# Optimization experiments

Hardware: AMD Instinct MI355X
Metric: run time of the kernel (lower is better)

## Reference

```python
import jax, jax.numpy as jnp
import numpy as np


def _cas(N):
    # Hartley cas matrix: cos(2*pi*k*n/N) + sin(2*pi*k*n/N), shape [N, N]
    n = jnp.arange(N, dtype=jnp.float32)
    ang = 2.0 * jnp.pi * n[:, None] * n[None, :] / N
    return jnp.cos(ang) + jnp.sin(ang)


def setup_inputs() -> dict:
    key = jax.random.key(0)
    k0, k1, k2, k3, k4 = jax.random.split(key, 5)
    B, N, C = 8, 4096, 768
    nb, bs, hf = 8, 96, 1
    scale = 0.02
    return {
        "x": jax.random.normal(k0, (B, N, C), jnp.float32),
        "w1": scale * jax.random.normal(k1, (2, nb, bs, bs * hf), jnp.float32),
        "b1": scale * jax.random.normal(k2, (2, nb, bs * hf), jnp.float32),
        "w2": scale * jax.random.normal(k3, (2, nb, bs * hf, bs), jnp.float32),
        "b2": scale * jax.random.normal(k4, (2, nb, bs), jnp.float32),
    }


def reference(x, w1, b1, w2, b2):
    SPARSITY = 0.01       # sparsity_threshold (softshrink lambda)
    FRAC = 1.0            # hard_thresholding_fraction
    B, N, C = x.shape
    H = W = int(np.sqrt(N))
    nb, bs = w1.shape[1], w1.shape[2]
    bias = x

    xf = x.astype(jnp.float32).reshape(B, H, W, C)
    cas = _cas(C)  # module's dht2d transforms the LAST (channel) dim
    xr = xf @ cas  # [B,H,W,C]; imag part is exactly zero after torch.complex(x, 0)
    xr = xr.reshape(B, H, W, nb, bs)

    # kept_modes = int((N//2+1)*frac), clamped by W-dim slicing semantics
    km = min(W, int((N // 2 + 1) * FRAC))

    # block-diagonal 2-layer MLP on (real, imag) with imag input == 0
    o1r = jax.nn.relu(jnp.einsum('bhwki,kio->bhwko', xr, w1[0]) + b1[0])
    o1i = jax.nn.relu(jnp.einsum('bhwki,kio->bhwko', xr, w1[1]) + b1[1])
    o2r = (jnp.einsum('bhwko,koc->bhwkc', o1r, w2[0])
           - jnp.einsum('bhwko,koc->bhwkc', o1i, w2[1]) + b2[0])
    o2i = (jnp.einsum('bhwko,koc->bhwkc', o1i, w2[0])
           + jnp.einsum('bhwko,koc->bhwkc', o1r, w2[1]) + b2[1])

    if km < W:
        mask = (jnp.arange(W) < km)[None, None, :, None, None]
        o2r = jnp.where(mask, o2r, 0.0)
        o2i = jnp.where(mask, o2i, 0.0)

    # softshrink on stacked real/imag
    ss = lambda v: jnp.sign(v) * jnp.maximum(jnp.abs(v) - SPARSITY, 0.0)
    o2r, o2i = ss(o2r), ss(o2i)

    real = o2r.reshape(B, H, W, C)
    imag = o2i.reshape(B, H, W, C)

    # idht2d: dht2d(complex) = real@cas - imag@cas, divided by TOTAL element count
    n_tot = B * H * W * C
    out = ((real - imag) @ cas) / n_tot
    out = out.reshape(B, N, C).astype(bias.dtype)
    return out + bias
```

## Files before the change

kernel.cpp:

```cpp
#include <hip/hip_runtime.h>
#include <hip/hip_bf16.h>
#include <cstdint>
#include <cstddef>

typedef __bf16 bf8_t __attribute__((ext_vector_type(8)));
typedef __bf16 bf4_t __attribute__((ext_vector_type(4)));
typedef float  f4_t  __attribute__((ext_vector_type(4)));

#define CC 768
#define NROWS 32768
#define NTOT 25165824

__device__ __forceinline__ void gld16(const void* g, void* l) {
  __builtin_amdgcn_global_load_lds(
      (const __attribute__((address_space(1))) void*)g,
      (__attribute__((address_space(3))) void*)l, 16, 0, 0);
}


__global__ void make_cas(__bf16* __restrict__ cas) {
  int idx = blockIdx.x * 256 + threadIdx.x;
  int i = idx / CC, j = idx - i * CC;
  int ij = (i * j) % CC;
  float ang = 6.283185307179586f * (float)ij / (float)CC;
  cas[idx] = (__bf16)(__cosf(ang) + __sinf(ang));
}

__global__ void cvt4(const float* __restrict__ x, __bf16* __restrict__ o) {
  int i = (blockIdx.x * 256 + threadIdx.x) * 4;
  float4 v = *(const float4*)(x + i);
  bf4_t r;
  r[0] = (__bf16)v.x; r[1] = (__bf16)v.y; r[2] = (__bf16)v.z; r[3] = (__bf16)v.w;
  *(bf4_t*)(o + i) = r;
}

__global__ void pack_w1(const float* __restrict__ w1, __bf16* __restrict__ w1f) {
  int f = blockIdx.x * 256 + threadIdx.x;
  int j = f & 7, lane = (f >> 3) & 63, rest = f >> 9;
  int nt = rest % 12, kt = (rest / 12) % 3, blk = rest / 36;
  int k = kt * 32 + (lane >> 4) * 8 + j;
  int o = nt * 16 + (lane & 15);
  float v = (o < 96) ? w1[(0 * 8 + blk) * 9216 + k * 96 + o]
                     : w1[(1 * 8 + blk) * 9216 + k * 96 + (o - 96)];
  w1f[f] = (__bf16)v;
}

__global__ void pack_w2(const float* __restrict__ w2, __bf16* __restrict__ w2f) {
  int f = blockIdx.x * 256 + threadIdx.x;
  int j = f & 7, lane = (f >> 3) & 63, rest = f >> 9;
  int nt = rest % 12, kt = (rest / 12) % 6, blk = rest / 72;
  int i = kt * 32 + (lane >> 4) * 8 + j;
  int o = nt * 16 + (lane & 15);
  float v;
  if (o < 96) v = (i < 96) ?  w2[(0 * 8 + blk) * 9216 + i * 96 + o]
                           : -w2[(1 * 8 + blk) * 9216 + (i - 96) * 96 + o];
  else        v = (i < 96) ?  w2[(1 * 8 + blk) * 9216 + i * 96 + (o - 96)]
                           :  w2[(0 * 8 + blk) * 9216 + (i - 96) * 96 + (o - 96)];
  w2f[f] = (__bf16)v;
}

__global__ __launch_bounds__(256, 2) void gemm_back(
    const __bf16* __restrict__ Zb, const __bf16* __restrict__ BT,
    float* __restrict__ Cf, const float* __restrict__ Xres, float scale)
{
  __shared__ __align__(16) char smem[49152];
  const int t = threadIdx.x;
  const int lane = t & 63, wid = t >> 6;
  const int wm = (wid >> 1) * 64, wn = (wid & 1) * 64;

  const int id = blockIdx.x;
  const int sid = (id & 7) * 192 + (id >> 3);
  const int m0 = (sid / 6) * 128, n0 = (sid % 6) * 128;

  const int q = lane >> 4, r = lane & 15;
  const __bf16* gA = Zb + (size_t)(m0 + (t >> 2)) * CC + (t & 3) * 8;
  const __bf16* gB = BT + (size_t)(n0 + (t >> 2)) * CC + (t & 3) * 8;
  const int ldsOff = (t >> 2) * 32 + (t & 3) * 8;

  auto stage = [&](int b, int tile) {
    int k0 = tile * 32;
    __bf16* lA = (__bf16*)(smem + b * 16384) + ldsOff;
    __bf16* lB = (__bf16*)(smem + b * 16384 + 8192) + ldsOff;
    gld16(gA + k0, lA);
    gld16(gA + (size_t)64 * CC + k0, lA + 64 * 32);
    gld16(gB + k0, lB);
    gld16(gB + (size_t)64 * CC + k0, lB + 64 * 32);
  };

  f4_t acc[4][4] = {};
  stage(0, 0);
  stage(1, 1);
  for (int tile = 0; tile < 24; ++tile) {
    int nt = tile + 2; if (nt > 23) nt = 23;
    stage((tile + 2) % 3, nt);
    asm volatile("s_waitcnt vmcnt(8)" ::: "memory");
    __builtin_amdgcn_s_barrier();
    const __bf16* sA = (const __bf16*)(smem + (tile % 3) * 16384);
    const __bf16* sB = sA + 8192 / 2;
    bf8_t af[4], bfr[4];
#pragma unroll
    for (int i = 0; i < 4; i++)
      af[i] = *(const bf8_t*)(sA + (wm + i * 16 + r) * 32 + q * 8);
#pragma unroll
    for (int j = 0; j < 4; j++)
      bfr[j] = *(const bf8_t*)(sB + (wn + j * 16 + r) * 32 + q * 8);
#pragma unroll
    for (int i = 0; i < 4; i++)
#pragma unroll
      for (int j = 0; j < 4; j++)
        acc[i][j] = __builtin_amdgcn_mfma_f32_16x16x32_bf16(af[i], bfr[j], acc[i][j], 0, 0, 0);
    __builtin_amdgcn_s_barrier();
  }

  float* cs = (float*)smem;
#pragma unroll
  for (int h = 0; h < 2; ++h) {
    __builtin_amdgcn_s_barrier();
    if ((wid >> 1) == h) {
#pragma unroll
      for (int i = 0; i < 4; i++)
#pragma unroll
        for (int j = 0; j < 4; j++)
#pragma unroll
          for (int rr = 0; rr < 4; rr++)
            cs[(i * 16 + q * 4 + rr) * 132 + wn + j * 16 + r] = acc[i][j][rr];
    }
    __builtin_amdgcn_s_barrier();
    const int u = t & 31, row8 = t >> 5;
#pragma unroll
    for (int p = 0; p < 8; ++p) {
      int rl = p * 8 + row8;
      size_t goff = (size_t)(m0 + h * 64 + rl) * CC + n0 + u * 4;
      f4_t xr = *(const f4_t*)(Xres + goff);
      f4_t cv = *(const f4_t*)(cs + rl * 132 + u * 4);
      f4_t o;
      o[0] = cv[0] * scale + xr[0];
      o[1] = cv[1] * scale + xr[1];
      o[2] = cv[2] * scale + xr[2];
      o[3] = cv[3] * scale + xr[3];
      *(f4_t*)(Cf + goff) = o;
    }
  }
}

__global__ __launch_bounds__(384, 3) void fused2(
    const __bf16* __restrict__ A, const __bf16* __restrict__ BT,
    const __bf16* __restrict__ w1f, const __bf16* __restrict__ w2f,
    const float* __restrict__ b1, const float* __restrict__ b2,
    __bf16* __restrict__ Z)
{
  __shared__ __align__(16) char smem[63488];
  __bf16* sA = (__bf16*)smem;
  __bf16* sB = (__bf16*)(smem + 8192);
  __bf16* Hs = (__bf16*)smem;
  __bf16* vt = (__bf16*)(smem + 25600);
  __bf16* zl = (__bf16*)(smem + 51200);

  const int t = threadIdx.x, lane = t & 63, w = t >> 6;
  const int id = blockIdx.x;
  const int sid = (id & 7) * 128 + (id >> 3);
  const int cbp = sid & 3;
  const int m0 = (sid >> 2) * 128;
  const int n0 = cbp * 192;
  const int q = lane >> 4, r = lane & 15;

  const __bf16* gA  = A  + (size_t)(m0 + (t >> 2)) * CC + (t & 3) * 8;
  const __bf16* gA2 = A  + (size_t)(m0 + 96 + (t >> 2)) * CC + (t & 3) * 8;
  const __bf16* gB  = BT + (size_t)(n0 + (t >> 2)) * CC + (t & 3) * 8;
  const __bf16* gB2 = BT + (size_t)(n0 + 96 + (t >> 2)) * CC + (t & 3) * 8;
  __bf16* lA  = sA + t * 8;
  __bf16* lA2 = sA + (384 + t) * 8;
  __bf16* lB  = sB + t * 8;
  __bf16* lB2 = sB + (384 + t) * 8;

  f4_t acc[8][2] = {};
  for (int k0 = 0; k0 < CC; k0 += 32) {
    __syncthreads();
    gld16(gA + k0, lA);
    if (t < 128) gld16(gA2 + k0, lA2);
    gld16(gB + k0, lB);
    gld16(gB2 + k0, lB2);
    __syncthreads();
    bf8_t af[8], bfr[2];
#pragma unroll
    for (int i = 0; i < 8; i++)
      af[i] = *(const bf8_t*)(sA + (i * 16 + r) * 32 + q * 8);
#pragma unroll
    for (int j = 0; j < 2; j++)
      bfr[j] = *(const bf8_t*)(sB + (w * 32 + j * 16 + r) * 32 + q * 8);
#pragma unroll
    for (int i = 0; i < 8; i++)
#pragma unroll
      for (int j = 0; j < 2; j++)
        acc[i][j] = __builtin_amdgcn_mfma_f32_16x16x32_bf16(af[i], bfr[j], acc[i][j], 0, 0, 0);
  }

#pragma unroll
  for (int h = 0; h < 2; h++) {
#pragma unroll
    for (int ii = 0; ii < 4; ii++)
#pragma unroll
      for (int j = 0; j < 2; j++) {
        int col = w * 32 + j * 16 + r;
#pragma unroll
        for (int rr = 0; rr < 4; rr++) {
          int row = ii * 16 + q * 4 + rr;
          vt[row * 200 + col] = (__bf16)acc[h * 4 + ii][j][rr];
        }
      }
    __syncthreads();

#pragma unroll
    for (int cb = 0; cb < 2; cb++) {
      const int bidx = cbp * 2 + cb;
      const __bf16* w1b = w1f + (size_t)bidx * (36 * 64 * 8);
      const __bf16* w2b = w2f + (size_t)bidx * (72 * 64 * 8);
      bf8_t w1r[3][2], w2r[6][2];
#pragma unroll
      for (int kt = 0; kt < 3; kt++)
#pragma unroll
        for (int j = 0; j < 2; j++)
          w1r[kt][j] = *(const bf8_t*)(w1b + ((size_t)(kt * 12 + 2 * w + j) * 64 + lane) * 8);
#pragma unroll
      for (int kt = 0; kt < 6; kt++) {
        w2r[kt][0] = *(const bf8_t*)(w2b + ((size_t)(kt * 12 + w) * 64 + lane) * 8);
        w2r[kt][1] = *(const bf8_t*)(w2b + ((size_t)(kt * 12 + w + 6) * 64 + lane) * 8);
      }
      float bb[2];
#pragma unroll
      for (int j = 0; j < 2; j++) {
        int c = (2 * w + j) * 16 + r;
        bb[j] = (c < 96) ? b1[bidx * 96 + c] : b1[768 + bidx * 96 + (c - 96)];
      }
      const float br = b2[bidx * 96 + w * 16 + r];
      const float bi = b2[768 + bidx * 96 + w * 16 + r];

#pragma unroll
      for (int rt = 0; rt < 4; rt++) {
        const __bf16* vp = vt + (rt * 16 + r) * 200 + cb * 96 + q * 8;
        f4_t a0 = {}, a1 = {};
#pragma unroll
        for (int kt = 0; kt < 3; kt++) {
          bf8_t a = *(const bf8_t*)(vp + kt * 32);
          a0 = __builtin_amdgcn_mfma_f32_16x16x32_bf16(a, w1r[kt][0], a0, 0, 0, 0);
          a1 = __builtin_amdgcn_mfma_f32_16x16x32_bf16(a, w1r[kt][1], a1, 0, 0, 0);
        }
#pragma unroll
        for (int j = 0; j < 2; j++) {
          int c = (2 * w + j) * 16 + r;
          f4_t* ap = j ? &a1 : &a0;
#pragma unroll
          for (int rr = 0; rr < 4; rr++) {
            float v = (*ap)[rr] + bb[j];
            Hs[(rt * 16 + q * 4 + rr) * 200 + c] = (__bf16)(v > 0.f ? v : 0.f);
          }
        }
      }
      __syncthreads();
#pragma unroll
      for (int rt = 0; rt < 4; rt++) {
        f4_t ar = {}, ai = {};
#pragma unroll
        for (int kt = 0; kt < 6; kt++) {
          bf8_t a = *(const bf8_t*)(&Hs[(rt * 16 + r) * 200 + kt * 32 + q * 8]);
          ar = __builtin_amdgcn_mfma_f32_16x16x32_bf16(a, w2r[kt][0], ar, 0, 0, 0);
          ai = __builtin_amdgcn_mfma_f32_16x16x32_bf16(a, w2r[kt][1], ai, 0, 0, 0);
        }
#pragma unroll
        for (int rr = 0; rr < 4; rr++) {
          float yr = ar[rr] + br, yi = ai[rr] + bi;
          float sr = fabsf(yr) - 0.01f; sr = sr > 0.f ? copysignf(sr, yr) : 0.f;
          float si = fabsf(yi) - 0.01f; si = si > 0.f ? copysignf(si, yi) : 0.f;
          zl[(rt * 16 + q * 4 + rr) * 96 + w * 16 + r] = (__bf16)(sr - si);
        }
      }
      __syncthreads();
      {
        const uint32_t* zsrc = (const uint32_t*)zl;
        int cdw = t % 48, crow = t / 48;
        int rbase = m0 + h * 64;
#pragma unroll
        for (int it = 0; it < 8; it++) {
          int row = it * 8 + crow;
          uint32_t* dst = (uint32_t*)(Z + (size_t)(rbase + row) * CC + n0 + cb * 96);
          dst[cdw] = zsrc[row * 48 + cdw];
        }
      }
    }
  }
}


extern "C" void kernel_launch(void* const* d_in, const int* in_sizes, int n_in,
                              void* d_out, int out_size, void* d_ws, size_t ws_size,
                              hipStream_t stream) {
  const float* x  = (const float*)d_in[0];
  const float* w1 = (const float*)d_in[1];
  const float* b1 = (const float*)d_in[2];
  const float* w2 = (const float*)d_in[3];
  const float* b2 = (const float*)d_in[4];
  float* out = (float*)d_out;

  char* ws = (char*)d_ws;
  size_t off = 0;
  auto alloc = [&](size_t bytes) {
    char* p = ws + off;
    off += (bytes + 255) & ~(size_t)255;
    return p;
  };
  __bf16* casb = (__bf16*)alloc((size_t)CC * CC * 2);
  __bf16* w1f  = (__bf16*)alloc((size_t)8 * 36 * 64 * 8 * 2);
  __bf16* w2f  = (__bf16*)alloc((size_t)8 * 72 * 64 * 8 * 2);
  __bf16* xb   = (__bf16*)alloc((size_t)NTOT * 2);
  __bf16* vv   = (__bf16*)alloc((size_t)NTOT * 2);

  make_cas<<<2304, 256, 0, stream>>>(casb);
  cvt4<<<24576, 256, 0, stream>>>(x, xb);
  pack_w1<<<576, 256, 0, stream>>>(w1, w1f);
  pack_w2<<<1152, 256, 0, stream>>>(w2, w2f);

  fused2<<<1024, 384, 0, stream>>>(xb, casb, w1f, w2f, b1, b2, vv);
  gemm_back<<<1536, 256, 0, stream>>>(vv, casb, out, x, 1.0f / 25165824.0f);
}
```

Before: 368.5 us.

## Triple-buffer the forward GEMM K-loop with async LDS loads and vmcnt waits

Replaces the single-buffer load/sync/compute loop in the fused forward kernel with a three-stage ring of LDS buffers (20 KB each) filled by global_load_lds two tiles ahead. Explicit s_waitcnt vmcnt thresholds plus raw barriers let the MFMA work on one tile overlap the global loads for later tiles, hiding memory latency. The three buffers fit within the existing 63 KB shared allocation. Redundant reloads of the last tile at the end of the loop and hand-tuned per-wave vmcnt counts add fragility.

Measured after the change: 340.9 us. 7.5% less time.

```diff
diff --git a/kernel.cpp b/kernel.cpp
--- a/kernel.cpp
+++ b/kernel.cpp
@@ -143,15 +143,13 @@
   }
 }
 
-__global__ __launch_bounds__(384, 3) void fused2(
+__global__ __launch_bounds__(384, 3) void fused3(
     const __bf16* __restrict__ A, const __bf16* __restrict__ BT,
     const __bf16* __restrict__ w1f, const __bf16* __restrict__ w2f,
     const float* __restrict__ b1, const float* __restrict__ b2,
     __bf16* __restrict__ Z)
 {
   __shared__ __align__(16) char smem[63488];
-  __bf16* sA = (__bf16*)smem;
-  __bf16* sB = (__bf16*)(smem + 8192);
   __bf16* Hs = (__bf16*)smem;
   __bf16* vt = (__bf16*)(smem + 25600);
   __bf16* zl = (__bf16*)(smem + 51200);
@@ -168,19 +166,27 @@
   const __bf16* gA2 = A  + (size_t)(m0 + 96 + (t >> 2)) * CC + (t & 3) * 8;
   const __bf16* gB  = BT + (size_t)(n0 + (t >> 2)) * CC + (t & 3) * 8;
   const __bf16* gB2 = BT + (size_t)(n0 + 96 + (t >> 2)) * CC + (t & 3) * 8;
-  __bf16* lA  = sA + t * 8;
-  __bf16* lA2 = sA + (384 + t) * 8;
-  __bf16* lB  = sB + t * 8;
-  __bf16* lB2 = sB + (384 + t) * 8;
+
+  auto stage = [&](int b, int tile) {
+    int k0 = tile * 32;
+    char* base = smem + b * 20480;
+    gld16(gA + k0, (__bf16*)base + t * 8);
+    if (t < 128) gld16(gA2 + k0, (__bf16*)base + (384 + t) * 8);
+    gld16(gB + k0, (__bf16*)(base + 8192) + t * 8);
+    gld16(gB2 + k0, (__bf16*)(base + 8192) + (384 + t) * 8);
+  };
 
   f4_t acc[8][2] = {};
-  for (int k0 = 0; k0 < CC; k0 += 32) {
-    __syncthreads();
-    gld16(gA + k0, lA);
-    if (t < 128) gld16(gA2 + k0, lA2);
-    gld16(gB + k0, lB);
-    gld16(gB2 + k0, lB2);
-    __syncthreads();
+  stage(0, 0);
+  stage(1, 1);
+  for (int tile = 0; tile < 24; ++tile) {
+    int nt = tile + 2; if (nt > 23) nt = 23;
+    stage((tile + 2) % 3, nt);
+    if (w < 2) asm volatile("s_waitcnt vmcnt(8)" ::: "memory");
+    else       asm volatile("s_waitcnt vmcnt(6)" ::: "memory");
+    __builtin_amdgcn_s_barrier();
+    const __bf16* sA = (const __bf16*)(smem + (tile % 3) * 20480);
+    const __bf16* sB = (const __bf16*)(smem + (tile % 3) * 20480 + 8192);
     bf8_t af[8], bfr[2];
 #pragma unroll
     for (int i = 0; i < 8; i++)
@@ -193,7 +199,10 @@
 #pragma unroll
       for (int j = 0; j < 2; j++)
         acc[i][j] = __builtin_amdgcn_mfma_f32_16x16x32_bf16(af[i], bfr[j], acc[i][j], 0, 0, 0);
+    __builtin_amdgcn_s_barrier();
   }
+  asm volatile("s_waitcnt vmcnt(0)" ::: "memory");
+  __builtin_amdgcn_s_barrier();
 
 #pragma unroll
   for (int h = 0; h < 2; h++) {
@@ -319,6 +328,6 @@
   pack_w1<<<576, 256, 0, stream>>>(w1, w1f);
   pack_w2<<<1152, 256, 0, stream>>>(w2, w2f);
 
-  fused2<<<1024, 384, 0, stream>>>(xb, casb, w1f, w2f, b1, b2, vv);
+  fused3<<<1024, 384, 0, stream>>>(xb, casb, w1f, w2f, b1, b2, vv);
   gemm_back<<<1536, 256, 0, stream>>>(vv, casb, out, x, 1.0f / 25165824.0f);
 }
```
